# Optimization experiments

Hardware: AMD Instinct MI355X
Metric: run time of the kernel (lower is better)

## Reference

```python
import jax, jax.numpy as jnp
from jax import lax
import numpy as np

# Dcls2_1d config (matches init_kwargs)
K_H, K_W = 3, 3          # base kernel size
DIL = 4                  # max dilation along dim 0 (learnable spacings)
LIM = DIL // 2           # each tap may move +/- LIM rows
KH_EFF = K_H + 2 * LIM   # constructed kernel height (7)
PAD_H = 1 + LIM          # user padding 1 adjusted by dilation//2 (as in _adjust_padding)
PAD_W = 1


def build_kernel(weight, P1):
    """Construct dense conv kernel by bilinear scatter of weights at
    continuous learnable row offsets P1. weight,P1: (O, I, K_H, K_W).
    Returns (O, I, KH_EFF, K_W)."""
    kh = jnp.arange(K_H, dtype=weight.dtype)[None, None, :, None]
    pos = kh + LIM + jnp.clip(P1, -LIM, LIM)      # continuous row position in [0, KH_EFF-1]
    p0 = jnp.floor(pos)
    frac = pos - p0                                # interpolation residual (grad flows to P)
    p0i = p0.astype(jnp.int32)
    oh0 = jax.nn.one_hot(p0i, KH_EFF, dtype=weight.dtype)        # (O,I,Kh,Kw,KH_EFF)
    oh1 = jax.nn.one_hot(p0i + 1, KH_EFF, dtype=weight.dtype)    # OOB rows -> all-zero row
    return (jnp.einsum('oihw,oihwk->oikw', weight * (1.0 - frac), oh0)
            + jnp.einsum('oihw,oihwk->oikw', weight * frac, oh1))


def setup_inputs() -> dict:
    key = jax.random.key(0)
    k1, k2, k3, k4 = jax.random.split(key, 4)
    x = jax.random.normal(k1, (16, 128, 64, 64), jnp.float32)
    weight = jax.random.normal(k2, (256, 128, 3, 3), jnp.float32) * 0.03
    bias = jax.random.normal(k3, (256,), jnp.float32) * 0.01
    # learnable positions span the allowed +/- LIM range to exercise interpolation
    P = jax.random.uniform(k4, (1, 256, 128, 3, 3), jnp.float32, -2.0, 2.0)
    return {"x": x, "weight": weight, "bias": bias, "P": P}


def reference(x, weight, bias, P):
    K = build_kernel(weight, P[0])
    out = lax.conv_general_dilated(
        x, K,
        window_strides=(1, 1),
        padding=((PAD_H, PAD_H), (PAD_W, PAD_W)),
        dimension_numbers=('NCHW', 'OIHW', 'NCHW'),
        feature_group_count=1)
    return out + bias[None, :, None, None]
```

## Files before the change

### kernel.cpp

```cpp
#include <hip/hip_runtime.h>
#include <hip/hip_bf16.h>

#define NIMG 16
#define CIN 128
#define COUT 256
#define HH 64
#define WW 64
#define KHE 7
#define KW_ 3
#define HP (HH + 6)
#define WP (WW + 2)
#define KDIM (CIN * KHE * KW_)
#define NKT 42

typedef __attribute__((ext_vector_type(8))) short short8;
typedef __attribute__((ext_vector_type(4))) float f32x4;

#define AS1(p) ((const __attribute__((address_space(1))) void*)(p))
#define AS3(p) ((__attribute__((address_space(3))) void*)(p))

__global__ void __launch_bounds__(256) pad_convert(const float* __restrict__ x,
                                                   ushort* __restrict__ xp) {
  const int bid = blockIdx.x;
  const int n = bid / HP, hp = bid % HP;
  const int h = hp - 3;
  ushort* dst = xp + (size_t)(n * HP + hp) * (WP * CIN);
  const int tid = threadIdx.x;

  if (h < 0 || h >= HH) {
    uint4* p = (uint4*)dst;
    uint4 z; z.x = z.y = z.z = z.w = 0u;
    for (int idx = tid; idx < (WP * CIN * 2) / 16; idx += 256) p[idx] = z;
    return;
  }

  __shared__ ushort t[CIN][WW + 1];
  for (int it = 0; it < (CIN * WW) / 256; ++it) {
    int flat = it * 256 + tid;
    int i = flat >> 6, w = flat & 63;
    float v = x[(((size_t)n * CIN + i) * HH + h) * WW + w];
    __hip_bfloat16 b = __float2bfloat16(v);
    t[i][w] = *(ushort*)&b;
  }
  __syncthreads();
  for (int it = 0; it < (WP * CIN) / 256; ++it) {
    int flat = it * 256 + tid;
    int wp = flat >> 7, i = flat & 127;
    int w = wp - 1;
    ushort v = (w < 0 || w >= WW) ? (ushort)0 : t[i][w];
    dst[flat] = v;
  }
}

__global__ void __launch_bounds__(256) build_kb(const float* __restrict__ weight,
                                                const float* __restrict__ P,
                                                ushort* __restrict__ kb) {
  int idx = blockIdx.x * 256 + threadIdx.x;
  if (idx >= COUT * KW_ * CIN) return;
  int i = idx & 127;
  int kw = (idx >> 7) % 3;
  int o = idx / (KW_ * CIN);
  int base = (o * CIN + i) * 9 + kw;

  float a[KHE] = {0.f, 0.f, 0.f, 0.f, 0.f, 0.f, 0.f};
#pragma unroll
  for (int kh = 0; kh < 3; ++kh) {
    float wv = weight[base + kh * 3];
    float p = P[base + kh * 3];
    p = fminf(2.f, fmaxf(-2.f, p));
    float pos = (float)(kh + 2) + p;
    float fl = floorf(pos);
    float fr = pos - fl;
    int r0 = (int)fl;
    float c0 = wv * (1.f - fr);
    float c1 = wv * fr;
#pragma unroll
    for (int r = 0; r < KHE; ++r) {
      a[r] += ((r0 == r) ? c0 : 0.f) + ((r0 + 1 == r) ? c1 : 0.f);
    }
  }
#pragma unroll
  for (int r = 0; r < KHE; ++r) {
    __hip_bfloat16 b = __float2bfloat16(a[r]);
    kb[((size_t)(o * KHE + r) * KW_ + kw) * CIN + i] = *(ushort*)&b;
  }
}

__global__ void __launch_bounds__(512, 2) dcls_gemm(const ushort* __restrict__ xp,
                                                    const ushort* __restrict__ kb,
                                                    const float* __restrict__ bias,
                                                    float* __restrict__ out) {
  __shared__ __align__(16) ushort As[2][256 * 64];
  __shared__ __align__(16) ushort Bs[2][256 * 64];

  const int tid = threadIdx.x;
  const int lane = tid & 63;
  const int wv = tid >> 6;
  const int wr = wv >> 2;
  const int wc = wv & 3;
  const int g = lane >> 4;
  const int lm = lane & 15;
  const int m0 = blockIdx.x << 8;

  const int srow = tid >> 3;
  const int swz = ((tid & 7) ^ (srow & 7)) * 8;

  const ushort* pA[4];
  const ushort* pB[4];
#pragma unroll
  for (int j = 0; j < 4; ++j) {
    int r = j * 64 + srow;
    int m = m0 + r;
    int ni = m >> 12, hh = (m >> 6) & 63, ww = m & 63;
    pA[j] = xp + (size_t)((ni * HP + hh) * WP + ww) * CIN + swz;
    pB[j] = kb + (size_t)r * KDIM + swz;
  }

#define STAGE(c, kt) do { \
    int kh_ = (kt) / 6; int rem_ = (kt) - kh_ * 6; \
    int kw2_ = rem_ >> 1; int ic_ = rem_ & 1; \
    int offA_ = (kh_ * WP + kw2_) * CIN + ic_ * 64; \
    int offB_ = (kh_ * KW_ + kw2_) * CIN + ic_ * 64; \
    _Pragma("unroll") \
    for (int j_ = 0; j_ < 4; ++j_) \
      __builtin_amdgcn_global_load_lds(AS1(pA[j_] + offA_), AS3(&As[c][(j_ * 64 + wv * 8) * 64]), 16, 0, 0); \
    _Pragma("unroll") \
    for (int j_ = 0; j_ < 4; ++j_) \
      __builtin_amdgcn_global_load_lds(AS1(pB[j_] + offB_), AS3(&Bs[c][(j_ * 64 + wv * 8) * 64]), 16, 0, 0); \
  } while (0)

  f32x4 acc[8][4] = {};
  const int swzR = (lm & 7) << 4;

  short8 bf[4];
  short8 af[4];

#define PHASE(Ab, Bb, mg, kk, READB) do { \
    if (READB) { \
      _Pragma("unroll") \
      for (int n_ = 0; n_ < 4; ++n_) { \
        int rowB_ = wc * 64 + n_ * 16 + lm; \
        bf[n_] = *(const short8*)((Bb) + rowB_ * 128 + (((kk) * 64 + g * 16) ^ swzR)); \
      } \
    } \
    _Pragma("unroll") \
    for (int m4_ = 0; m4_ < 4; ++m4_) { \
      int rowA_ = wr * 128 + (mg) * 64 + m4_ * 16 + lm; \
      af[m4_] = *(const short8*)((Ab) + rowA_ * 128 + (((kk) * 64 + g * 16) ^ swzR)); \
    } \
    __builtin_amdgcn_sched_barrier(0); \
    __builtin_amdgcn_s_barrier(); \
    asm volatile("s_waitcnt lgkmcnt(0)" ::: "memory"); \
    __builtin_amdgcn_sched_barrier(0); \
    __builtin_amdgcn_s_setprio(1); \
    _Pragma("unroll") \
    for (int m4_ = 0; m4_ < 4; ++m4_) \
      _Pragma("unroll") \
      for (int n_ = 0; n_ < 4; ++n_) \
        acc[(mg) * 4 + m4_][n_] = __builtin_amdgcn_mfma_f32_16x16x32_bf16( \
            af[m4_], bf[n_], acc[(mg) * 4 + m4_][n_], 0, 0, 0); \
    __builtin_amdgcn_s_setprio(0); \
    __builtin_amdgcn_s_barrier(); \
  } while (0)

  STAGE(0, 0);
  STAGE(1, 1);
  asm volatile("s_waitcnt vmcnt(8)" ::: "memory");
  __builtin_amdgcn_sched_barrier(0);
  __builtin_amdgcn_s_barrier();

  for (int kt = 0; kt < NKT; ++kt) {
    const int c = kt & 1;
    const char* Ab = (const char*)&As[c][0];
    const char* Bb = (const char*)&Bs[c][0];

    PHASE(Ab, Bb, 0, 0, 1);
    PHASE(Ab, Bb, 1, 0, 0);
    PHASE(Ab, Bb, 0, 1, 1);
    PHASE(Ab, Bb, 1, 1, 0);

    if (kt < NKT - 1) {
      __builtin_amdgcn_sched_barrier(0);
      if (kt + 2 < NKT) {
        STAGE(c, kt + 2);
        asm volatile("s_waitcnt vmcnt(8)" ::: "memory");
      } else {
        asm volatile("s_waitcnt vmcnt(0)" ::: "memory");
      }
      __builtin_amdgcn_sched_barrier(0);
      __builtin_amdgcn_s_barrier();
    }
  }
#undef PHASE
#undef STAGE

#pragma unroll
  for (int fn = 0; fn < 4; ++fn) {
    int o = wc * 64 + fn * 16 + lm;
    float bv = bias[o];
#pragma unroll
    for (int fm = 0; fm < 8; ++fm) {
      int m = m0 + wr * 128 + fm * 16 + g * 4;
      int ni = m >> 12, hh = (m >> 6) & 63, ww = m & 63;
      f32x4 v = acc[fm][fn];
      v[0] += bv; v[1] += bv; v[2] += bv; v[3] += bv;
      *(f32x4*)(out + (size_t)((ni * COUT + o) * HH + hh) * WW + ww) = v;
    }
  }
}

extern "C" void kernel_launch(void* const* d_in, const int* in_sizes, int n_in,
                              void* d_out, int out_size, void* d_ws, size_t ws_size,
                              hipStream_t stream) {
  const float* x = (const float*)d_in[0];
  const float* weight = (const float*)d_in[1];
  const float* bias = (const float*)d_in[2];
  const float* P = (const float*)d_in[3];
  float* out = (float*)d_out;

  const size_t xp_elems = (size_t)NIMG * HP * WP * CIN;
  ushort* xp = (ushort*)d_ws;
  ushort* kb = (ushort*)((char*)d_ws + xp_elems * 2);

  hipLaunchKernelGGL(pad_convert, dim3(NIMG * HP), dim3(256), 0, stream, x, xp);
  hipLaunchKernelGGL(build_kb, dim3((COUT * KW_ * CIN + 255) / 256), dim3(256), 0, stream,
                     weight, P, kb);
  hipLaunchKernelGGL(dcls_gemm, dim3(65536 / 256), dim3(512), 0, stream, xp, kb, bias, out);
}
```

Before: 114.3 us.

## Load B fragments directly from global into registers, drop B LDS staging

Rewrites the weight layout in build_kb into k-slice-major fragment order so each lane can load its MFMA B operand straight from global memory into registers, double-buffered across k-tiles. The B shared-memory buffers and their staging loads are removed, which halves LDS use and cuts the number of LDS reads and barriers per k-tile. The MFMA inner loop is regrouped to process both k-halves per half-tile with fewer barriers. The cost is more register pressure from the 16 extra short8 B fragments and global-load latency that must be covered by the prefetch distance. It also relies on the weights being served from cache, since every block now rereads them from global memory.

```diff
diff --git a/kernel.cpp b/kernel.cpp
--- a/kernel.cpp
+++ b/kernel.cpp
@@ -12,6 +12,7 @@
 #define WP (WW + 2)
 #define KDIM (CIN * KHE * KW_)
 #define NKT 42
+#define NKSLICE (NKT * 2)
 
 typedef __attribute__((ext_vector_type(8))) short short8;
 typedef __attribute__((ext_vector_type(4))) float f32x4;
@@ -54,7 +55,7 @@
 
 __global__ void __launch_bounds__(256) build_kb(const float* __restrict__ weight,
                                                 const float* __restrict__ P,
-                                                ushort* __restrict__ kb) {
+                                                ushort* __restrict__ kb2) {
   int idx = blockIdx.x * 256 + threadIdx.x;
   if (idx >= COUT * KW_ * CIN) return;
   int i = idx & 127;
@@ -82,16 +83,16 @@
 #pragma unroll
   for (int r = 0; r < KHE; ++r) {
     __hip_bfloat16 b = __float2bfloat16(a[r]);
-    kb[((size_t)(o * KHE + r) * KW_ + kw) * CIN + i] = *(ushort*)&b;
+    int kslice = (r * 3 + kw) * 4 + (i >> 5);
+    kb2[(size_t)kslice * 8192 + o * 32 + (i & 31)] = *(ushort*)&b;
   }
 }
 
 __global__ void __launch_bounds__(512, 2) dcls_gemm(const ushort* __restrict__ xp,
-                                                    const ushort* __restrict__ kb,
+                                                    const ushort* __restrict__ kb2,
                                                     const float* __restrict__ bias,
                                                     float* __restrict__ out) {
   __shared__ __align__(16) ushort As[2][256 * 64];
-  __shared__ __align__(16) ushort Bs[2][256 * 64];
 
   const int tid = threadIdx.x;
   const int lane = tid & 63;
@@ -106,93 +107,86 @@
   const int swz = ((tid & 7) ^ (srow & 7)) * 8;
 
   const ushort* pA[4];
-  const ushort* pB[4];
 #pragma unroll
   for (int j = 0; j < 4; ++j) {
     int r = j * 64 + srow;
     int m = m0 + r;
     int ni = m >> 12, hh = (m >> 6) & 63, ww = m & 63;
     pA[j] = xp + (size_t)((ni * HP + hh) * WP + ww) * CIN + swz;
-    pB[j] = kb + (size_t)r * KDIM + swz;
-  }
-
-#define STAGE(c, kt) do { \
+  }
+
+  const ushort* kbB = kb2 + (size_t)wc * 2048 + lm * 32 + g * 8;
+
+#define STAGEA(c, kt) do { \
     int kh_ = (kt) / 6; int rem_ = (kt) - kh_ * 6; \
     int kw2_ = rem_ >> 1; int ic_ = rem_ & 1; \
     int offA_ = (kh_ * WP + kw2_) * CIN + ic_ * 64; \
-    int offB_ = (kh_ * KW_ + kw2_) * CIN + ic_ * 64; \
     _Pragma("unroll") \
     for (int j_ = 0; j_ < 4; ++j_) \
       __builtin_amdgcn_global_load_lds(AS1(pA[j_] + offA_), AS3(&As[c][(j_ * 64 + wv * 8) * 64]), 16, 0, 0); \
+  } while (0)
+
+#define LOADB(dst, kt) do { \
     _Pragma("unroll") \
-    for (int j_ = 0; j_ < 4; ++j_) \
-      __builtin_amdgcn_global_load_lds(AS1(pB[j_] + offB_), AS3(&Bs[c][(j_ * 64 + wv * 8) * 64]), 16, 0, 0); \
+    for (int n_ = 0; n_ < 4; ++n_) \
+      _Pragma("unroll") \
+      for (int kk_ = 0; kk_ < 2; ++kk_) \
+        dst[n_][kk_] = *(const short8*)(kbB + (size_t)((kt) * 2 + kk_) * 8192 + n_ * 512); \
   } while (0)
 
   f32x4 acc[8][4] = {};
   const int swzR = (lm & 7) << 4;
 
-  short8 bf[4];
-  short8 af[4];
-
-#define PHASE(Ab, Bb, mg, kk, READB) do { \
-    if (READB) { \
+  short8 bf0[4][2], bf1[4][2];
+
+#define TILE_MFMA(c, bf) do { \
+    const char* Ab = (const char*)&As[c][0]; \
+    _Pragma("unroll") \
+    for (int half_ = 0; half_ < 2; ++half_) { \
+      short8 af[4][2]; \
       _Pragma("unroll") \
-      for (int n_ = 0; n_ < 4; ++n_) { \
-        int rowB_ = wc * 64 + n_ * 16 + lm; \
-        bf[n_] = *(const short8*)((Bb) + rowB_ * 128 + (((kk) * 64 + g * 16) ^ swzR)); \
-      } \
+      for (int m4_ = 0; m4_ < 4; ++m4_) \
+        _Pragma("unroll") \
+        for (int kk_ = 0; kk_ < 2; ++kk_) { \
+          int rowA_ = wr * 128 + half_ * 64 + m4_ * 16 + lm; \
+          af[m4_][kk_] = *(const short8*)(Ab + rowA_ * 128 + ((kk_ * 64 + g * 16) ^ swzR)); \
+        } \
+      _Pragma("unroll") \
+      for (int kk_ = 0; kk_ < 2; ++kk_) \
+        _Pragma("unroll") \
+        for (int m4_ = 0; m4_ < 4; ++m4_) \
+          _Pragma("unroll") \
+          for (int n_ = 0; n_ < 4; ++n_) \
+            acc[half_ * 4 + m4_][n_] = __builtin_amdgcn_mfma_f32_16x16x32_bf16( \
+                af[m4_][kk_], bf[n_][kk_], acc[half_ * 4 + m4_][n_], 0, 0, 0); \
     } \
-    _Pragma("unroll") \
-    for (int m4_ = 0; m4_ < 4; ++m4_) { \
-      int rowA_ = wr * 128 + (mg) * 64 + m4_ * 16 + lm; \
-      af[m4_] = *(const short8*)((Ab) + rowA_ * 128 + (((kk) * 64 + g * 16) ^ swzR)); \
-    } \
+  } while (0)
+
+#define SUBITER(kt, c, bfc) do { \
+    asm volatile("s_waitcnt vmcnt(12)" ::: "memory"); \
+    __builtin_amdgcn_s_barrier(); \
     __builtin_amdgcn_sched_barrier(0); \
+    TILE_MFMA(c, bfc); \
+    int ktn_ = ((kt) + 2 < NKT) ? (kt) + 2 : 0; \
+    LOADB(bfc, ktn_); \
     __builtin_amdgcn_s_barrier(); \
-    asm volatile("s_waitcnt lgkmcnt(0)" ::: "memory"); \
     __builtin_amdgcn_sched_barrier(0); \
-    __builtin_amdgcn_s_setprio(1); \
-    _Pragma("unroll") \
-    for (int m4_ = 0; m4_ < 4; ++m4_) \
-      _Pragma("unroll") \
-      for (int n_ = 0; n_ < 4; ++n_) \
-        acc[(mg) * 4 + m4_][n_] = __builtin_amdgcn_mfma_f32_16x16x32_bf16( \
-            af[m4_], bf[n_], acc[(mg) * 4 + m4_][n_], 0, 0, 0); \
-    __builtin_amdgcn_s_setprio(0); \
-    __builtin_amdgcn_s_barrier(); \
-  } while (0)
-
-  STAGE(0, 0);
-  STAGE(1, 1);
-  asm volatile("s_waitcnt vmcnt(8)" ::: "memory");
-  __builtin_amdgcn_sched_barrier(0);
-  __builtin_amdgcn_s_barrier();
-
-  for (int kt = 0; kt < NKT; ++kt) {
-    const int c = kt & 1;
-    const char* Ab = (const char*)&As[c][0];
-    const char* Bb = (const char*)&Bs[c][0];
-
-    PHASE(Ab, Bb, 0, 0, 1);
-    PHASE(Ab, Bb, 1, 0, 0);
-    PHASE(Ab, Bb, 0, 1, 1);
-    PHASE(Ab, Bb, 1, 1, 0);
-
-    if (kt < NKT - 1) {
-      __builtin_amdgcn_sched_barrier(0);
-      if (kt + 2 < NKT) {
-        STAGE(c, kt + 2);
-        asm volatile("s_waitcnt vmcnt(8)" ::: "memory");
-      } else {
-        asm volatile("s_waitcnt vmcnt(0)" ::: "memory");
-      }
-      __builtin_amdgcn_sched_barrier(0);
-      __builtin_amdgcn_s_barrier();
-    }
-  }
-#undef PHASE
-#undef STAGE
+    STAGEA(c, ktn_); \
+  } while (0)
+
+  STAGEA(0, 0);
+  LOADB(bf0, 0);
+  STAGEA(1, 1);
+  LOADB(bf1, 1);
+
+  for (int kt = 0; kt < NKT; kt += 2) {
+    SUBITER(kt, 0, bf0);
+    SUBITER(kt + 1, 1, bf1);
+  }
+#undef SUBITER
+#undef TILE_MFMA
+#undef LOADB
+#undef STAGEA
 
 #pragma unroll
   for (int fn = 0; fn < 4; ++fn) {
@@ -220,10 +214,10 @@
 
   const size_t xp_elems = (size_t)NIMG * HP * WP * CIN;
   ushort* xp = (ushort*)d_ws;
-  ushort* kb = (ushort*)((char*)d_ws + xp_elems * 2);
+  ushort* kb2 = (ushort*)((char*)d_ws + xp_elems * 2);
 
   hipLaunchKernelGGL(pad_convert, dim3(NIMG * HP), dim3(256), 0, stream, x, xp);
   hipLaunchKernelGGL(build_kb, dim3((COUT * KW_ * CIN + 255) / 256), dim3(256), 0, stream,
-                     weight, P, kb);
-  hipLaunchKernelGGL(dcls_gemm, dim3(65536 / 256), dim3(512), 0, stream, xp, kb, bias, out);
-}
+                     weight, P, kb2);
+  hipLaunchKernelGGL(dcls_gemm, dim3(65536 / 256), dim3(512), 0, stream, xp, kb2, bias, out);
+}
```

Result: faster. 99.55 us (-12.9%).

## Restructure GEMM into 16-wave blocks with k-chunk-major LDS and prelaid weights

Applied to the files above, without the earlier changes.

The GEMM kernel now runs 1024 threads (16 waves in a 4x4 grid, each owning a 64x64 output tile) instead of 8 waves owning 128x64 tiles. build_kb writes the weights in a k-chunk-major layout that matches the shared-memory fragment layout, so the XOR swizzle and the per-phase barriers disappear. Block indices are remapped to group neighbouring M-tiles for L2 reuse, and the K loop visits kh fastest. The cost is a shallower prefetch: each iteration waits on vmcnt(0) for a single-stage prefetch, which may expose more global-load latency than the old two-deep pipeline.

```diff
diff --git a/kernel.cpp b/kernel.cpp
--- a/kernel.cpp
+++ b/kernel.cpp
@@ -54,7 +54,7 @@
 
 __global__ void __launch_bounds__(256) build_kb(const float* __restrict__ weight,
                                                 const float* __restrict__ P,
-                                                ushort* __restrict__ kb) {
+                                                ushort* __restrict__ kb3) {
   int idx = blockIdx.x * 256 + threadIdx.x;
   if (idx >= COUT * KW_ * CIN) return;
   int i = idx & 127;
@@ -79,119 +79,103 @@
       a[r] += ((r0 == r) ? c0 : 0.f) + ((r0 + 1 == r) ? c1 : 0.f);
     }
   }
+  int ic = i >> 6, kl = i & 63, kc = kl >> 3, e = kl & 7;
 #pragma unroll
   for (int r = 0; r < KHE; ++r) {
     __hip_bfloat16 b = __float2bfloat16(a[r]);
-    kb[((size_t)(o * KHE + r) * KW_ + kw) * CIN + i] = *(ushort*)&b;
-  }
-}
-
-__global__ void __launch_bounds__(512, 2) dcls_gemm(const ushort* __restrict__ xp,
-                                                    const ushort* __restrict__ kb,
-                                                    const float* __restrict__ bias,
-                                                    float* __restrict__ out) {
-  __shared__ __align__(16) ushort As[2][256 * 64];
-  __shared__ __align__(16) ushort Bs[2][256 * 64];
+    int kt = ic * 21 + kw * 7 + r;
+    kb3[((size_t)(kt * 8 + kc) * 256 + o) * 8 + e] = *(ushort*)&b;
+  }
+}
+
+__global__ void __launch_bounds__(1024, 4) dcls_gemm(const ushort* __restrict__ xp,
+                                                     const ushort* __restrict__ kb3,
+                                                     const float* __restrict__ bias,
+                                                     float* __restrict__ out) {
+  __shared__ __align__(16) ushort As[2][16384];
+  __shared__ __align__(16) ushort Bs[2][16384];
 
   const int tid = threadIdx.x;
   const int lane = tid & 63;
-  const int wv = tid >> 6;
-  const int wr = wv >> 2;
-  const int wc = wv & 3;
+  const int w = tid >> 6;
+  const int wr = w >> 2;
+  const int wc = w & 3;
   const int g = lane >> 4;
   const int lm = lane & 15;
-  const int m0 = blockIdx.x << 8;
-
-  const int srow = tid >> 3;
-  const int swz = ((tid & 7) ^ (srow & 7)) * 8;
-
-  const ushort* pA[4];
-  const ushort* pB[4];
-#pragma unroll
-  for (int j = 0; j < 4; ++j) {
-    int r = j * 64 + srow;
-    int m = m0 + r;
+
+  const int bid = blockIdx.x;
+  const int mt = (bid & 7) * 32 + (bid >> 3);
+  const int m0 = mt << 8;
+
+  const ushort* pA[2];
+  const ushort* pB[2];
+#pragma unroll
+  for (int j = 0; j < 2; ++j) {
+    int c = j * 16 + w;
+    int row = ((c & 3) << 6) + lane;
+    int m = m0 + row;
     int ni = m >> 12, hh = (m >> 6) & 63, ww = m & 63;
-    pA[j] = xp + (size_t)((ni * HP + hh) * WP + ww) * CIN + swz;
-    pB[j] = kb + (size_t)r * KDIM + swz;
-  }
-
-#define STAGE(c, kt) do { \
-    int kh_ = (kt) / 6; int rem_ = (kt) - kh_ * 6; \
-    int kw2_ = rem_ >> 1; int ic_ = rem_ & 1; \
-    int offA_ = (kh_ * WP + kw2_) * CIN + ic_ * 64; \
-    int offB_ = (kh_ * KW_ + kw2_) * CIN + ic_ * 64; \
+    pA[j] = xp + (size_t)((ni * HP + hh) * WP + ww) * CIN + (c >> 2) * 8;
+    pB[j] = kb3 + (size_t)(c * 64 + lane) * 8;
+  }
+
+#define STAGE(buf, kt) do { \
+    int kh_ = (kt) % 7; int kw_ = ((kt) / 7) % 3; int ic_ = (kt) / 21; \
+    int offA_ = (kh_ * WP + kw_) * CIN + ic_ * 64; \
+    size_t offB_ = (size_t)(kt) * 16384; \
     _Pragma("unroll") \
-    for (int j_ = 0; j_ < 4; ++j_) \
-      __builtin_amdgcn_global_load_lds(AS1(pA[j_] + offA_), AS3(&As[c][(j_ * 64 + wv * 8) * 64]), 16, 0, 0); \
+    for (int j_ = 0; j_ < 2; ++j_) { \
+      __builtin_amdgcn_global_load_lds(AS1(pA[j_] + offA_), \
+          AS3(&As[buf][(j_ * 16 + w) * 512]), 16, 0, 0); \
+      __builtin_amdgcn_global_load_lds(AS1(pB[j_] + offB_), \
+          AS3(&Bs[buf][(j_ * 16 + w) * 512]), 16, 0, 0); \
+    } \
+  } while (0)
+
+  f32x4 acc[4][4] = {};
+
+  const int kcOff = g << 12;
+  const int rowA = ((wr << 6) + lm) << 4;
+  const int rowB = ((wc << 6) + lm) << 4;
+
+  short8 af[4], bf[4];
+
+#define KKSTEP(Ab, Bb, kk) do { \
     _Pragma("unroll") \
-    for (int j_ = 0; j_ < 4; ++j_) \
-      __builtin_amdgcn_global_load_lds(AS1(pB[j_] + offB_), AS3(&Bs[c][(j_ * 64 + wv * 8) * 64]), 16, 0, 0); \
-  } while (0)
-
-  f32x4 acc[8][4] = {};
-  const int swzR = (lm & 7) << 4;
-
-  short8 bf[4];
-  short8 af[4];
-
-#define PHASE(Ab, Bb, mg, kk, READB) do { \
-    if (READB) { \
-      _Pragma("unroll") \
-      for (int n_ = 0; n_ < 4; ++n_) { \
-        int rowB_ = wc * 64 + n_ * 16 + lm; \
-        bf[n_] = *(const short8*)((Bb) + rowB_ * 128 + (((kk) * 64 + g * 16) ^ swzR)); \
-      } \
-    } \
-    _Pragma("unroll") \
-    for (int m4_ = 0; m4_ < 4; ++m4_) { \
-      int rowA_ = wr * 128 + (mg) * 64 + m4_ * 16 + lm; \
-      af[m4_] = *(const short8*)((Ab) + rowA_ * 128 + (((kk) * 64 + g * 16) ^ swzR)); \
+    for (int f_ = 0; f_ < 4; ++f_) { \
+      af[f_] = *(const short8*)((Ab) + (kk) * 16384 + kcOff + rowA + f_ * 256); \
+      bf[f_] = *(const short8*)((Bb) + (kk) * 16384 + kcOff + rowB + f_ * 256); \
     } \
     __builtin_amdgcn_sched_barrier(0); \
-    __builtin_amdgcn_s_barrier(); \
     asm volatile("s_waitcnt lgkmcnt(0)" ::: "memory"); \
     __builtin_amdgcn_sched_barrier(0); \
     __builtin_amdgcn_s_setprio(1); \
     _Pragma("unroll") \
-    for (int m4_ = 0; m4_ < 4; ++m4_) \
+    for (int mf_ = 0; mf_ < 4; ++mf_) \
       _Pragma("unroll") \
-      for (int n_ = 0; n_ < 4; ++n_) \
-        acc[(mg) * 4 + m4_][n_] = __builtin_amdgcn_mfma_f32_16x16x32_bf16( \
-            af[m4_], bf[n_], acc[(mg) * 4 + m4_][n_], 0, 0, 0); \
+      for (int nf_ = 0; nf_ < 4; ++nf_) \
+        acc[mf_][nf_] = __builtin_amdgcn_mfma_f32_16x16x32_bf16( \
+            af[mf_], bf[nf_], acc[mf_][nf_], 0, 0, 0); \
     __builtin_amdgcn_s_setprio(0); \
-    __builtin_amdgcn_s_barrier(); \
   } while (0)
 
   STAGE(0, 0);
-  STAGE(1, 1);
-  asm volatile("s_waitcnt vmcnt(8)" ::: "memory");
-  __builtin_amdgcn_sched_barrier(0);
-  __builtin_amdgcn_s_barrier();
 
   for (int kt = 0; kt < NKT; ++kt) {
-    const int c = kt & 1;
-    const char* Ab = (const char*)&As[c][0];
-    const char* Bb = (const char*)&Bs[c][0];
-
-    PHASE(Ab, Bb, 0, 0, 1);
-    PHASE(Ab, Bb, 1, 0, 0);
-    PHASE(Ab, Bb, 0, 1, 1);
-    PHASE(Ab, Bb, 1, 1, 0);
-
-    if (kt < NKT - 1) {
-      __builtin_amdgcn_sched_barrier(0);
-      if (kt + 2 < NKT) {
-        STAGE(c, kt + 2);
-        asm volatile("s_waitcnt vmcnt(8)" ::: "memory");
-      } else {
-        asm volatile("s_waitcnt vmcnt(0)" ::: "memory");
-      }
-      __builtin_amdgcn_sched_barrier(0);
-      __builtin_amdgcn_s_barrier();
+    __builtin_amdgcn_sched_barrier(0);
+    asm volatile("s_waitcnt vmcnt(0)" ::: "memory");
+    __builtin_amdgcn_s_barrier();
+    __builtin_amdgcn_sched_barrier(0);
+    {
+      int ktn = (kt + 1 < NKT) ? kt + 1 : 0;
+      STAGE((kt + 1) & 1, ktn);
     }
-  }
-#undef PHASE
+    const char* Ab = (const char*)&As[kt & 1][0];
+    const char* Bb = (const char*)&Bs[kt & 1][0];
+    KKSTEP(Ab, Bb, 0);
+    KKSTEP(Ab, Bb, 1);
+  }
+#undef KKSTEP
 #undef STAGE
 
 #pragma unroll
@@ -199,8 +183,8 @@
     int o = wc * 64 + fn * 16 + lm;
     float bv = bias[o];
 #pragma unroll
-    for (int fm = 0; fm < 8; ++fm) {
-      int m = m0 + wr * 128 + fm * 16 + g * 4;
+    for (int fm = 0; fm < 4; ++fm) {
+      int m = m0 + wr * 64 + fm * 16 + g * 4;
       int ni = m >> 12, hh = (m >> 6) & 63, ww = m & 63;
       f32x4 v = acc[fm][fn];
       v[0] += bv; v[1] += bv; v[2] += bv; v[3] += bv;
@@ -220,10 +204,10 @@
 
   const size_t xp_elems = (size_t)NIMG * HP * WP * CIN;
   ushort* xp = (ushort*)d_ws;
-  ushort* kb = (ushort*)((char*)d_ws + xp_elems * 2);
+  ushort* kb3 = (ushort*)((char*)d_ws + xp_elems * 2);
 
   hipLaunchKernelGGL(pad_convert, dim3(NIMG * HP), dim3(256), 0, stream, x, xp);
   hipLaunchKernelGGL(build_kb, dim3((COUT * KW_ * CIN + 255) / 256), dim3(256), 0, stream,
-                     weight, P, kb);
-  hipLaunchKernelGGL(dcls_gemm, dim3(65536 / 256), dim3(512), 0, stream, xp, kb, bias, out);
-}
+                     weight, P, kb3);
+  hipLaunchKernelGGL(dcls_gemm, dim3(256), dim3(1024), 0, stream, xp, kb3, bias, out);
+}
```

Measured after the change: 134.6 us. +17.8%, slower.
